# Optimization experiments

Hardware: AMD Instinct MI355X
Metric: run time of the kernel (lower is better)

## Reference

```python
import jax, jax.numpy as jnp
import numpy as np

N = 100000
E = 1600000
P = 500000
IN_C = 128
HID = 128


def _sage_conv(x, edge_index, w_l, b_l, w_r):
    # PyG SAGEConv (aggr='mean'): out = lin_l(mean_{j->i} x_j) + lin_r(x_i)
    src, dst = edge_index[0], edge_index[1]
    msg = x[src]                                    # [E, C] gather
    agg = jax.ops.segment_sum(msg, dst, num_segments=N)        # [N, C]
    deg = jax.ops.segment_sum(jnp.ones((src.shape[0],), x.dtype), dst, num_segments=N)
    mean = agg / jnp.clip(deg, 1.0)[:, None]
    return mean @ w_l + b_l + x @ w_r


def setup_inputs() -> dict:
    key = jax.random.key(0)
    ks = jax.random.split(key, 12)
    s_in = 1.0 / np.sqrt(IN_C)
    s_h = 1.0 / np.sqrt(HID)
    s_2h = 1.0 / np.sqrt(2 * HID)
    return {
        "x": jax.random.normal(ks[0], (N, IN_C), jnp.float32),
        "w1_l": jax.random.uniform(ks[1], (IN_C, HID), jnp.float32, -s_in, s_in),
        "b1": jax.random.uniform(ks[2], (HID,), jnp.float32, -s_in, s_in),
        "w1_r": jax.random.uniform(ks[3], (IN_C, HID), jnp.float32, -s_in, s_in),
        "w2_l": jax.random.uniform(ks[4], (HID, HID), jnp.float32, -s_h, s_h),
        "b2": jax.random.uniform(ks[5], (HID,), jnp.float32, -s_h, s_h),
        "w2_r": jax.random.uniform(ks[6], (HID, HID), jnp.float32, -s_h, s_h),
        "wd1": jax.random.uniform(ks[7], (2 * HID, HID), jnp.float32, -s_2h, s_2h),
        "bd1": jax.random.uniform(ks[8], (HID,), jnp.float32, -s_2h, s_2h),
        "wd2": jax.random.uniform(ks[9], (HID, 1), jnp.float32, -s_h, s_h),
        "bd2": jax.random.uniform(ks[10], (1,), jnp.float32, -s_h, s_h),
        "edge_index": jax.random.randint(ks[11], (2, E), 0, N, jnp.int64),
        "edge_pairs": jax.random.randint(jax.random.fold_in(key, 99), (2, P), 0, N, jnp.int64),
    }


def reference(x, w1_l, b1, w1_r, w2_l, b2, w2_r, wd1, bd1, wd2, bd2, edge_index, edge_pairs):
    # encode: two SAGEConv layers with ReLU between
    h = jax.nn.relu(_sage_conv(x, edge_index, w1_l, b1, w1_r))
    h = _sage_conv(h, edge_index, w2_l, b2, w2_r)
    # decode: gather endpoints, concat, 2-layer MLP, squeeze
    feat = jnp.concatenate([h[edge_pairs[0]], h[edge_pairs[1]]], axis=1)  # [P, 2H]
    out = jax.nn.relu(feat @ wd1 + bd1) @ wd2 + bd2
    return out.squeeze(-1)
```

## Files before the change

kernel.cpp:

```cpp
#include <hip/hip_runtime.h>
#include <hip/hip_bf16.h>

#define NN 100000
#define NE 1600000
#define NP 500000
#define C 128
#define NBUCK 782

typedef __attribute__((ext_vector_type(8))) short bf16x8;
typedef __attribute__((ext_vector_type(4))) float f32x4;
typedef _Float16 f16;
typedef __attribute__((ext_vector_type(4))) _Float16 f16x4;
typedef __attribute__((ext_vector_type(8))) _Float16 f16x8;

__device__ inline unsigned short bfbits(float x) {
    __hip_bfloat16 h = __float2bfloat16(x);
    union { __hip_bfloat16 h; unsigned short u; } v; v.h = h;
    return v.u;
}
__device__ inline float bf2f(unsigned short b) {
    return __uint_as_float(((unsigned)b) << 16);
}

__device__ inline void split8core(const float* xs, bf16x8& hi, bf16x8& lo) {
    union { unsigned short s[8]; bf16x8 v; } uh, ul;
#pragma unroll
    for (int j = 0; j < 8; ++j) {
        unsigned short h = bfbits(xs[j]);
        uh.s[j] = h;
        ul.s[j] = bfbits(xs[j] - bf2f(h));
    }
    hi = uh.v;
    lo = ul.v;
}

__device__ inline void split8(const float* p, bf16x8& hi, bf16x8& lo) {
    f32x4 a = *(const f32x4*)p;
    f32x4 b = *(const f32x4*)(p + 4);
    float xs[8] = {a.x, a.y, a.z, a.w, b.x, b.y, b.z, b.w};
    split8core(xs, hi, lo);
}

__device__ inline void split8h(const f16* p, bf16x8& hi, bf16x8& lo) {
    f16x8 v = *(const f16x8*)p;
    float xs[8];
#pragma unroll
    for (int j = 0; j < 8; ++j) xs[j] = (float)v[j];
    split8core(xs, hi, lo);
}

__global__ __launch_bounds__(256) void f32_to_f16_kernel(
        const float* __restrict__ in, f16* __restrict__ out, int n4) {
    int i = blockIdx.x * 256 + threadIdx.x;
    if (i < n4) {
        float4 v = *(const float4*)&in[i * 4];
        f16x4 h = {(f16)v.x, (f16)v.y, (f16)v.z, (f16)v.w};
        *(f16x4*)&out[i * 4] = h;
    }
}

__global__ __launch_bounds__(256) void bin_count_kernel(
        const int* __restrict__ dst, int* __restrict__ gcnt, int nE) {
    __shared__ int h[NBUCK];
    int tid = threadIdx.x;
    for (int i = tid; i < NBUCK; i += 256) h[i] = 0;
    __syncthreads();
    int base = blockIdx.x * 8192;
#pragma unroll
    for (int j = 0; j < 32; ++j) {
        int e = base + tid + j * 256;
        if (e < nE) atomicAdd(&h[dst[e] >> 7], 1);
    }
    __syncthreads();
    for (int i = tid; i < NBUCK; i += 256)
        if (h[i]) atomicAdd(&gcnt[i], h[i]);
}

__global__ __launch_bounds__(1024) void bin_scan_kernel(
        const int* __restrict__ gcnt, int* __restrict__ gstart,
        int* __restrict__ gcursor) {
    __shared__ int s[1024];
    int tid = threadIdx.x;
    int v = (tid < NBUCK) ? gcnt[tid] : 0;
    s[tid] = v;
    __syncthreads();
    for (int off = 1; off < 1024; off <<= 1) {
        int t = (tid >= off) ? s[tid - off] : 0;
        __syncthreads();
        s[tid] += t;
        __syncthreads();
    }
    int excl = s[tid] - v;
    if (tid < NBUCK) { gstart[tid] = excl; gcursor[tid] = excl; }
    if (tid == NBUCK - 1) gstart[NBUCK] = excl + v;
}

__global__ __launch_bounds__(256) void bin_scatter_kernel(
        const int* __restrict__ src, const int* __restrict__ dst,
        int* __restrict__ gcursor, unsigned* __restrict__ elist, int nE) {
    __shared__ unsigned stage[4096];
    __shared__ unsigned short sbkt[4096];
    __shared__ int h[NBUCK];
    __shared__ int ex[NBUCK];
    __shared__ int gb[NBUCK];
    __shared__ int psum[256];
    int tid = threadIdx.x;
    for (int i = tid; i < NBUCK; i += 256) h[i] = 0;
    __syncthreads();
    int base = blockIdx.x * 4096;
    unsigned pk[16]; int bk[16];
#pragma unroll
    for (int j = 0; j < 16; ++j) {
        int e = base + tid + j * 256;
        bool ok = e < nE;
        int d = ok ? dst[e] : 0;
        int s = ok ? src[e] : 0;
        bk[j] = ok ? (d >> 7) : -1;
        pk[j] = ((unsigned)(d & 127) << 17) | (unsigned)s;
        if (ok) atomicAdd(&h[bk[j]], 1);
    }
    __syncthreads();
    int lo = tid * 4;
    int c4[4]; int sum = 0;
#pragma unroll
    for (int j = 0; j < 4; ++j) {
        int idx = lo + j;
        c4[j] = (idx < NBUCK) ? h[idx] : 0;
        sum += c4[j];
    }
    psum[tid] = sum;
    __syncthreads();
    for (int off = 1; off < 256; off <<= 1) {
        int t = (tid >= off) ? psum[tid - off] : 0;
        __syncthreads();
        psum[tid] += t;
        __syncthreads();
    }
    int run = psum[tid] - sum;
#pragma unroll
    for (int j = 0; j < 4; ++j) {
        int idx = lo + j;
        if (idx < NBUCK) ex[idx] = run;
        run += c4[j];
    }
    __syncthreads();
    for (int i = tid; i < NBUCK; i += 256)
        if (h[i] > 0) gb[i] = atomicAdd(&gcursor[i], h[i]);
    for (int i = tid; i < NBUCK; i += 256) h[i] = 0;
    __syncthreads();
#pragma unroll
    for (int j = 0; j < 16; ++j) {
        if (bk[j] >= 0) {
            int r = ex[bk[j]] + atomicAdd(&h[bk[j]], 1);
            stage[r] = pk[j];
            sbkt[r] = (unsigned short)bk[j];
        }
    }
    __syncthreads();
    int tot = min(4096, nE - base);
    for (int i = tid; i < tot; i += 256) {
        int b = sbkt[i];
        elist[gb[b] + (i - ex[b])] = stage[i];
    }
}

__global__ __launch_bounds__(256) void bucket_csr_kernel(
        const unsigned* __restrict__ elist, const int* __restrict__ gstart,
        int* __restrict__ ssrc, int* __restrict__ offs) {
    __shared__ int cnt[128];
    __shared__ int sc[128];
    int tid = threadIdx.x;
    int b = blockIdx.x;
    if (tid < 128) cnt[tid] = 0;
    __syncthreads();
    int s = gstart[b], e = gstart[b + 1];
    for (int i = s + tid; i < e; i += 256)
        atomicAdd(&cnt[(elist[i] >> 17) & 127], 1);
    __syncthreads();
    int v = 0;
    if (tid < 128) { v = cnt[tid]; sc[tid] = v; }
    __syncthreads();
    for (int off = 1; off < 128; off <<= 1) {
        int t = 0;
        if (tid < 128 && tid >= off) t = sc[tid - off];
        __syncthreads();
        if (tid < 128) sc[tid] += t;
        __syncthreads();
    }
    if (tid < 128) {
        int start = s + sc[tid] - v;
        cnt[tid] = start;
        int node = b * 128 + tid;
        if (node < NN) offs[node] = start;
    }
    if (b == NBUCK - 1 && tid == 0) offs[NN] = NE;
    __syncthreads();
    for (int i = s + tid; i < e; i += 256) {
        unsigned p = elist[i];
        int r = (p >> 17) & 127;
        int pos = atomicAdd(&cnt[r], 1);
        ssrc[pos] = (int)(p & 0x1FFFF);
    }
}

__global__ void compose_kernel(const float* __restrict__ w2l, const float* __restrict__ w2r,
                               const float* __restrict__ b2,
                               const float* __restrict__ wd1, const float* __restrict__ bd1,
                               float* __restrict__ wcomp, float* __restrict__ bcomp) {
    int c = threadIdx.x;
    int k = blockIdx.x;
    if (k < C) {
        float wma = 0, wmb = 0, wha = 0, whb = 0;
        for (int j = 0; j < C; ++j) {
            float wt = wd1[j * C + c];
            float wb = wd1[(C + j) * C + c];
            float l = w2l[k * C + j];
            float r = w2r[k * C + j];
            wma += l * wt; wmb += l * wb;
            wha += r * wt; whb += r * wb;
        }
        wcomp[0 * C * C + k * C + c] = wma;
        wcomp[1 * C * C + k * C + c] = wha;
        wcomp[2 * C * C + k * C + c] = wmb;
        wcomp[3 * C * C + k * C + c] = whb;
    } else {
        float ba = bd1[c], bb = 0;
        for (int j = 0; j < C; ++j) {
            float bj = b2[j];
            ba += bj * wd1[j * C + c];
            bb += bj * wd1[(C + j) * C + c];
        }
        bcomp[c] = ba;
        bcomp[C + c] = bb;
    }
}

__global__ void pack_w1_kernel(const float* __restrict__ wl, const float* __restrict__ wr,
                               short* __restrict__ Wh, short* __restrict__ Wl) {
    int t = blockIdx.x * 256 + threadIdx.x;
    int j = t & 7, l = (t >> 3) & 63;
    int kf = (t >> 9) & 7;
    int nf = t >> 12;
    int k = kf * 32 + ((l >> 4) << 3) + j;
    int n = nf * 16 + (l & 15);
    float w = (k < C) ? wl[k * C + n] : wr[(k - C) * C + n];
    unsigned short h = bfbits(w);
    Wh[t] = (short)h;
    Wl[t] = (short)bfbits(w - bf2f(h));
}

__global__ void pack_w2_kernel(const float* __restrict__ wcomp,
                               short* __restrict__ Wh, short* __restrict__ Wl) {
    int t = blockIdx.x * 256 + threadIdx.x;
    int j = t & 7, l = (t >> 3) & 63;
    int kf = (t >> 9) & 7;
    int nf = t >> 12;
    int k = kf * 32 + ((l >> 4) << 3) + j;
    int n = nf * 16 + (l & 15);
    int sel = (k >= C ? 1 : 0) + (n >= C ? 2 : 0);
    float w = wcomp[sel * C * C + (k & (C - 1)) * C + (n & (C - 1))];
    unsigned short h = bfbits(w);
    Wh[t] = (short)h;
    Wl[t] = (short)bfbits(w - bf2f(h));
}

__global__ __launch_bounds__(256) void gather_mean_f16_kernel(
        const f16* __restrict__ xin, const int* __restrict__ offs,
        const int* __restrict__ ssrc, f16* __restrict__ mean) {
    int gid = blockIdx.x * 256 + threadIdx.x;
    int hw = gid >> 5;
    int lane = threadIdx.x & 31;
    int nhw = (gridDim.x * 256) >> 5;
    for (int n = hw; n < NN; n += nhw) {
        int start = offs[n];
        int end = offs[n + 1];
        float4 acc = make_float4(0.f, 0.f, 0.f, 0.f);
        int e = start;
        for (; e + 7 < end; e += 8) {
            f16x4 v[8];
#pragma unroll
            for (int u = 0; u < 8; ++u)
                v[u] = *(const f16x4*)(xin + (size_t)ssrc[e + u] * C + lane * 4);
#pragma unroll
            for (int u = 0; u < 8; ++u) {
                acc.x += (float)v[u][0]; acc.y += (float)v[u][1];
                acc.z += (float)v[u][2]; acc.w += (float)v[u][3];
            }
        }
        for (; e < end; ++e) {
            f16x4 v = *(const f16x4*)(xin + (size_t)ssrc[e] * C + lane * 4);
            acc.x += (float)v[0]; acc.y += (float)v[1];
            acc.z += (float)v[2]; acc.w += (float)v[3];
        }
        float inv = 1.0f / fmaxf((float)(end - start), 1.0f);
        f16x4 m = {(f16)(acc.x * inv), (f16)(acc.y * inv),
                   (f16)(acc.z * inv), (f16)(acc.w * inv)};
        *(f16x4*)(mean + (size_t)n * C + lane * 4) = m;
    }
}

template<int MS, int NF, int RELU, int A1F16>
__global__ __launch_bounds__(256, 4) void mfma_transform_kernel(
        const f16* A0, const void* A1v,
        const short* __restrict__ Bh, const short* __restrict__ Bl,
        const float* __restrict__ bias,
        f16* O0, f16* O1) {
    constexpr int KF = 8;
    int tid = threadIdx.x;
    int w = tid >> 6, l = tid & 63;
    int m0 = blockIdx.x * (64 * MS) + w * (MS * 16);
    int lr = l & 15;
    int lk = (l >> 4) * 8;

    f32x4 acc[MS][NF];
#pragma unroll
    for (int ms = 0; ms < MS; ++ms)
#pragma unroll
        for (int nf = 0; nf < NF; ++nf)
            acc[ms][nf] = (f32x4){0.0f, 0.0f, 0.0f, 0.0f};

    const bf16x8* Bhp = (const bf16x8*)Bh;
    const bf16x8* Blp = (const bf16x8*)Bl;

#pragma unroll
    for (int kf = 0; kf < KF; ++kf) {
        int kofs = (kf & 3) * 32 + lk;
        bf16x8 ah[MS], al[MS];
#pragma unroll
        for (int ms = 0; ms < MS; ++ms) {
            int r = m0 + ms * 16 + lr;
            r = (r < NN) ? r : (NN - 1);
            if (kf < 4) {
                split8h(A0 + (size_t)r * C + kofs, ah[ms], al[ms]);
            } else if (A1F16) {
                split8h((const f16*)A1v + (size_t)r * C + kofs, ah[ms], al[ms]);
            } else {
                split8((const float*)A1v + (size_t)r * C + kofs, ah[ms], al[ms]);
            }
        }
#pragma unroll
        for (int nf = 0; nf < NF; ++nf) {
            bf16x8 bh = Bhp[(nf * KF + kf) * 64 + l];
            bf16x8 bl = Blp[(nf * KF + kf) * 64 + l];
#pragma unroll
            for (int ms = 0; ms < MS; ++ms) {
                acc[ms][nf] = __builtin_amdgcn_mfma_f32_16x16x32_bf16(ah[ms], bh, acc[ms][nf], 0, 0, 0);
                acc[ms][nf] = __builtin_amdgcn_mfma_f32_16x16x32_bf16(al[ms], bh, acc[ms][nf], 0, 0, 0);
                acc[ms][nf] = __builtin_amdgcn_mfma_f32_16x16x32_bf16(ah[ms], bl, acc[ms][nf], 0, 0, 0);
            }
        }
    }

#pragma unroll
    for (int nf = 0; nf < NF; ++nf) {
        int col = nf * 16 + lr;
        float bv = bias[col];
        f16* O = (NF == 8) ? O0 : ((nf < 8) ? O0 : O1);
        int c = (nf & 7) * 16 + lr;
#pragma unroll
        for (int ms = 0; ms < MS; ++ms) {
#pragma unroll
            for (int i = 0; i < 4; ++i) {
                int r = m0 + ms * 16 + (l >> 4) * 4 + i;
                if (r < NN) {
                    float v = acc[ms][nf][i] + bv;
                    if (RELU) v = fmaxf(v, 0.0f);
                    O[(size_t)r * C + c] = (f16)v;
                }
            }
        }
    }
}

__global__ __launch_bounds__(256) void decode_kernel(
        const f16* __restrict__ a, const f16* __restrict__ b,
        const int* __restrict__ pu, const int* __restrict__ pv,
        const float* __restrict__ wd2, const float* __restrict__ bd2,
        float* __restrict__ out) {
    int gid = blockIdx.x * 256 + threadIdx.x;
    int hw = gid >> 5;
    int lane = threadIdx.x & 31;
    int nhw = (gridDim.x * 256) >> 5;
    float4 w2 = *(const float4*)&wd2[lane * 4];
    float bout = bd2[0];
    for (int p = hw; p < NP; p += 2 * nhw) {
        int p2 = p + nhw;
        bool ok2 = p2 < NP;
        int u1 = pu[p], v1 = pv[p];
        int u2 = ok2 ? pu[p2] : 0, v2 = ok2 ? pv[p2] : 0;
        f16x4 a1 = *(const f16x4*)(a + (size_t)u1 * C + lane * 4);
        f16x4 b1 = *(const f16x4*)(b + (size_t)v1 * C + lane * 4);
        f16x4 a2 = *(const f16x4*)(a + (size_t)u2 * C + lane * 4);
        f16x4 b2 = *(const f16x4*)(b + (size_t)v2 * C + lane * 4);
        float s1 = fmaxf((float)a1[0] + (float)b1[0], 0.0f) * w2.x
                 + fmaxf((float)a1[1] + (float)b1[1], 0.0f) * w2.y
                 + fmaxf((float)a1[2] + (float)b1[2], 0.0f) * w2.z
                 + fmaxf((float)a1[3] + (float)b1[3], 0.0f) * w2.w;
        float s2 = fmaxf((float)a2[0] + (float)b2[0], 0.0f) * w2.x
                 + fmaxf((float)a2[1] + (float)b2[1], 0.0f) * w2.y
                 + fmaxf((float)a2[2] + (float)b2[2], 0.0f) * w2.z
                 + fmaxf((float)a2[3] + (float)b2[3], 0.0f) * w2.w;
#pragma unroll
        for (int off = 16; off; off >>= 1) {
            s1 += __shfl_down(s1, off, 32);
            s2 += __shfl_down(s2, off, 32);
        }
        if (lane == 0) {
            out[p] = s1 + bout;
            if (ok2) out[p2] = s2 + bout;
        }
    }
}

extern "C" void kernel_launch(void* const* d_in, const int* in_sizes, int n_in,
                              void* d_out, int out_size, void* d_ws, size_t ws_size,
                              hipStream_t stream) {
    const float* x    = (const float*)d_in[0];
    const float* w1_l = (const float*)d_in[1];
    const float* b1   = (const float*)d_in[2];
    const float* w1_r = (const float*)d_in[3];
    const float* w2_l = (const float*)d_in[4];
    const float* b2   = (const float*)d_in[5];
    const float* w2_r = (const float*)d_in[6];
    const float* wd1  = (const float*)d_in[7];
    const float* bd1  = (const float*)d_in[8];
    const float* wd2  = (const float*)d_in[9];
    const float* bd2  = (const float*)d_in[10];
    const int* edge_index = (const int*)d_in[11];
    const int* edge_pairs = (const int*)d_in[12];

    const int* esrc = edge_index;
    const int* edst = edge_index + NE;
    const int* pu = edge_pairs;
    const int* pv = edge_pairs + NP;

    int* gcnt    = (int*)d_ws;
    int* gstart  = gcnt + 1024;
    int* gcursor = gstart + 1024;
    int* offs    = gcursor + 1024;
    unsigned* elist = (unsigned*)(offs + ((NN + 1 + 255) & ~255));
    int* ssrc    = (int*)(elist + NE);
    f16* xh      = (f16*)(ssrc + ((NE + 255) & ~255));
    f16* mean_h  = xh + (size_t)NN * C;
    f16* h1h     = mean_h + (size_t)NN * C;
    f16* a_h     = h1h + (size_t)NN * C;
    f16* b_h     = a_h + (size_t)NN * C;
    float* wcomp = (float*)(b_h + (size_t)NN * C);
    float* bcomp = wcomp + 4 * C * C;
    short* w1h = (short*)(bcomp + 2 * C);
    short* w1l = w1h + 256 * 128;
    short* w2h = w1l + 256 * 128;
    short* w2l = w2h + 256 * 256;

    hipMemsetAsync(gcnt, 0, sizeof(int) * 1024, stream);

    bin_count_kernel<<<(NE + 8191) / 8192, 256, 0, stream>>>(edst, gcnt, NE);
    bin_scan_kernel<<<1, 1024, 0, stream>>>(gcnt, gstart, gcursor);
    bin_scatter_kernel<<<(NE + 4095) / 4096, 256, 0, stream>>>(esrc, edst, gcursor, elist, NE);
    bucket_csr_kernel<<<NBUCK, 256, 0, stream>>>(elist, gstart, ssrc, offs);

    compose_kernel<<<C + 1, C, 0, stream>>>(w2_l, w2_r, b2, wd1, bd1, wcomp, bcomp);
    pack_w1_kernel<<<128, 256, 0, stream>>>(w1_l, w1_r, w1h, w1l);
    pack_w2_kernel<<<256, 256, 0, stream>>>(wcomp, w2h, w2l);

    f32_to_f16_kernel<<<(NN * C / 4 + 255) / 256, 256, 0, stream>>>(x, xh, NN * C / 4);

    gather_mean_f16_kernel<<<6144, 256, 0, stream>>>(xh, offs, ssrc, mean_h);
    mfma_transform_kernel<2, 8, 1, 0><<<(NN + 127) / 128, 256, 0, stream>>>(
        mean_h, (const void*)x, w1h, w1l, b1, h1h, nullptr);
    gather_mean_f16_kernel<<<6144, 256, 0, stream>>>(h1h, offs, ssrc, mean_h);
    mfma_transform_kernel<1, 16, 0, 1><<<(NN + 63) / 64, 256, 0, stream>>>(
        mean_h, (const void*)h1h, w2h, w2l, bcomp, a_h, b_h);

    decode_kernel<<<4096, 256, 0, stream>>>(a_h, b_h, pu, pv, wd2, bd2, (float*)d_out);
}
```

Measured before the change: 380.1 us.

## Switch transform GEMMs to f16 MFMA with split weights and 2D tiling

The dense transform kernels now feed the f16 activations straight into f16 MFMA instructions, dropping the per-element bf16 hi/lo split of the A operand. Only the weights keep a hi/lo f16 split, so each tile issues two MFMAs instead of three. The first layer reads the f16 copy of x instead of the f32 input. The tiling also changes to 4 row fragments by 4 column fragments per wave, with the output columns spread across blockIdx.y. This cuts ALU conversion work and MFMA count, but it re-reads the A rows once per column block and loses the lo-part correction on activations, which may affect accuracy.

```diff
diff --git a/kernel.cpp b/kernel.cpp
--- a/kernel.cpp
+++ b/kernel.cpp
@@ -7,47 +7,10 @@
 #define C 128
 #define NBUCK 782
 
-typedef __attribute__((ext_vector_type(8))) short bf16x8;
 typedef __attribute__((ext_vector_type(4))) float f32x4;
 typedef _Float16 f16;
 typedef __attribute__((ext_vector_type(4))) _Float16 f16x4;
 typedef __attribute__((ext_vector_type(8))) _Float16 f16x8;
-
-__device__ inline unsigned short bfbits(float x) {
-    __hip_bfloat16 h = __float2bfloat16(x);
-    union { __hip_bfloat16 h; unsigned short u; } v; v.h = h;
-    return v.u;
-}
-__device__ inline float bf2f(unsigned short b) {
-    return __uint_as_float(((unsigned)b) << 16);
-}
-
-__device__ inline void split8core(const float* xs, bf16x8& hi, bf16x8& lo) {
-    union { unsigned short s[8]; bf16x8 v; } uh, ul;
-#pragma unroll
-    for (int j = 0; j < 8; ++j) {
-        unsigned short h = bfbits(xs[j]);
-        uh.s[j] = h;
-        ul.s[j] = bfbits(xs[j] - bf2f(h));
-    }
-    hi = uh.v;
-    lo = ul.v;
-}
-
-__device__ inline void split8(const float* p, bf16x8& hi, bf16x8& lo) {
-    f32x4 a = *(const f32x4*)p;
-    f32x4 b = *(const f32x4*)(p + 4);
-    float xs[8] = {a.x, a.y, a.z, a.w, b.x, b.y, b.z, b.w};
-    split8core(xs, hi, lo);
-}
-
-__device__ inline void split8h(const f16* p, bf16x8& hi, bf16x8& lo) {
-    f16x8 v = *(const f16x8*)p;
-    float xs[8];
-#pragma unroll
-    for (int j = 0; j < 8; ++j) xs[j] = (float)v[j];
-    split8core(xs, hi, lo);
-}
 
 __global__ __launch_bounds__(256) void f32_to_f16_kernel(
         const float* __restrict__ in, f16* __restrict__ out, int n4) {
@@ -236,7 +199,7 @@
 }
 
 __global__ void pack_w1_kernel(const float* __restrict__ wl, const float* __restrict__ wr,
-                               short* __restrict__ Wh, short* __restrict__ Wl) {
+                               f16* __restrict__ Wh, f16* __restrict__ Wl) {
     int t = blockIdx.x * 256 + threadIdx.x;
     int j = t & 7, l = (t >> 3) & 63;
     int kf = (t >> 9) & 7;
@@ -244,13 +207,13 @@
     int k = kf * 32 + ((l >> 4) << 3) + j;
     int n = nf * 16 + (l & 15);
     float w = (k < C) ? wl[k * C + n] : wr[(k - C) * C + n];
-    unsigned short h = bfbits(w);
-    Wh[t] = (short)h;
-    Wl[t] = (short)bfbits(w - bf2f(h));
+    f16 h = (f16)w;
+    Wh[t] = h;
+    Wl[t] = (f16)(w - (float)h);
 }
 
 __global__ void pack_w2_kernel(const float* __restrict__ wcomp,
-                               short* __restrict__ Wh, short* __restrict__ Wl) {
+                               f16* __restrict__ Wh, f16* __restrict__ Wl) {
     int t = blockIdx.x * 256 + threadIdx.x;
     int j = t & 7, l = (t >> 3) & 63;
     int kf = (t >> 9) & 7;
@@ -259,9 +222,9 @@
     int n = nf * 16 + (l & 15);
     int sel = (k >= C ? 1 : 0) + (n >= C ? 2 : 0);
     float w = wcomp[sel * C * C + (k & (C - 1)) * C + (n & (C - 1))];
-    unsigned short h = bfbits(w);
-    Wh[t] = (short)h;
-    Wl[t] = (short)bfbits(w - bf2f(h));
+    f16 h = (f16)w;
+    Wh[t] = h;
+    Wl[t] = (f16)(w - (float)h);
 }
 
 __global__ __launch_bounds__(256) void gather_mean_f16_kernel(
@@ -299,16 +262,19 @@
     }
 }
 
-template<int MS, int NF, int RELU, int A1F16>
-__global__ __launch_bounds__(256, 4) void mfma_transform_kernel(
-        const f16* A0, const void* A1v,
-        const short* __restrict__ Bh, const short* __restrict__ Bl,
+template<int NFT, int RELU>
+__global__ __launch_bounds__(256, 4) void mfma_transform_f16_kernel(
+        const f16* __restrict__ A0, const f16* __restrict__ A1,
+        const f16* __restrict__ Bh, const f16* __restrict__ Bl,
         const float* __restrict__ bias,
         f16* O0, f16* O1) {
     constexpr int KF = 8;
+    constexpr int MS = 4;
+    constexpr int NF = 4;
     int tid = threadIdx.x;
     int w = tid >> 6, l = tid & 63;
     int m0 = blockIdx.x * (64 * MS) + w * (MS * 16);
+    int nf0 = blockIdx.y * NF;
     int lr = l & 15;
     int lk = (l >> 4) * 8;
 
@@ -319,44 +285,38 @@
         for (int nf = 0; nf < NF; ++nf)
             acc[ms][nf] = (f32x4){0.0f, 0.0f, 0.0f, 0.0f};
 
-    const bf16x8* Bhp = (const bf16x8*)Bh;
-    const bf16x8* Blp = (const bf16x8*)Bl;
+    const f16x8* Bhp = (const f16x8*)Bh;
+    const f16x8* Blp = (const f16x8*)Bl;
 
 #pragma unroll
     for (int kf = 0; kf < KF; ++kf) {
+        const f16* Asrc = (kf < 4) ? A0 : A1;
         int kofs = (kf & 3) * 32 + lk;
-        bf16x8 ah[MS], al[MS];
+        f16x8 a[MS];
 #pragma unroll
         for (int ms = 0; ms < MS; ++ms) {
             int r = m0 + ms * 16 + lr;
             r = (r < NN) ? r : (NN - 1);
-            if (kf < 4) {
-                split8h(A0 + (size_t)r * C + kofs, ah[ms], al[ms]);
-            } else if (A1F16) {
-                split8h((const f16*)A1v + (size_t)r * C + kofs, ah[ms], al[ms]);
-            } else {
-                split8((const float*)A1v + (size_t)r * C + kofs, ah[ms], al[ms]);
+            a[ms] = *(const f16x8*)(Asrc + (size_t)r * C + kofs);
+        }
+#pragma unroll
+        for (int nf = 0; nf < NF; ++nf) {
+            f16x8 bh = Bhp[((nf0 + nf) * KF + kf) * 64 + l];
+            f16x8 bl = Blp[((nf0 + nf) * KF + kf) * 64 + l];
+#pragma unroll
+            for (int ms = 0; ms < MS; ++ms) {
+                acc[ms][nf] = __builtin_amdgcn_mfma_f32_16x16x32_f16(a[ms], bh, acc[ms][nf], 0, 0, 0);
+                acc[ms][nf] = __builtin_amdgcn_mfma_f32_16x16x32_f16(a[ms], bl, acc[ms][nf], 0, 0, 0);
             }
         }
-#pragma unroll
-        for (int nf = 0; nf < NF; ++nf) {
-            bf16x8 bh = Bhp[(nf * KF + kf) * 64 + l];
-            bf16x8 bl = Blp[(nf * KF + kf) * 64 + l];
-#pragma unroll
-            for (int ms = 0; ms < MS; ++ms) {
-                acc[ms][nf] = __builtin_amdgcn_mfma_f32_16x16x32_bf16(ah[ms], bh, acc[ms][nf], 0, 0, 0);
-                acc[ms][nf] = __builtin_amdgcn_mfma_f32_16x16x32_bf16(al[ms], bh, acc[ms][nf], 0, 0, 0);
-                acc[ms][nf] = __builtin_amdgcn_mfma_f32_16x16x32_bf16(ah[ms], bl, acc[ms][nf], 0, 0, 0);
-            }
-        }
     }
 
 #pragma unroll
     for (int nf = 0; nf < NF; ++nf) {
-        int col = nf * 16 + lr;
-        float bv = bias[col];
-        f16* O = (NF == 8) ? O0 : ((nf < 8) ? O0 : O1);
-        int c = (nf & 7) * 16 + lr;
+        int nfg = nf0 + nf;
+        float bv = bias[nfg * 16 + lr];
+        f16* O = (NFT == 8) ? O0 : ((nfg < 8) ? O0 : O1);
+        int c = ((NFT == 8) ? nfg : (nfg & 7)) * 16 + lr;
 #pragma unroll
         for (int ms = 0; ms < MS; ++ms) {
 #pragma unroll
@@ -447,10 +407,10 @@
     f16* b_h     = a_h + (size_t)NN * C;
     float* wcomp = (float*)(b_h + (size_t)NN * C);
     float* bcomp = wcomp + 4 * C * C;
-    short* w1h = (short*)(bcomp + 2 * C);
-    short* w1l = w1h + 256 * 128;
-    short* w2h = w1l + 256 * 128;
-    short* w2l = w2h + 256 * 256;
+    f16* w1h = (f16*)(bcomp + 2 * C);
+    f16* w1l = w1h + 256 * 128;
+    f16* w2h = w1l + 256 * 128;
+    f16* w2l = w2h + 256 * 256;
 
     hipMemsetAsync(gcnt, 0, sizeof(int) * 1024, stream);
 
@@ -465,12 +425,13 @@
 
     f32_to_f16_kernel<<<(NN * C / 4 + 255) / 256, 256, 0, stream>>>(x, xh, NN * C / 4);
 
+    int rblocks = (NN + 255) / 256;
     gather_mean_f16_kernel<<<6144, 256, 0, stream>>>(xh, offs, ssrc, mean_h);
-    mfma_transform_kernel<2, 8, 1, 0><<<(NN + 127) / 128, 256, 0, stream>>>(
-        mean_h, (const void*)x, w1h, w1l, b1, h1h, nullptr);
+    mfma_transform_f16_kernel<8, 1><<<dim3(rblocks, 2), 256, 0, stream>>>(
+        mean_h, xh, w1h, w1l, b1, h1h, nullptr);
     gather_mean_f16_kernel<<<6144, 256, 0, stream>>>(h1h, offs, ssrc, mean_h);
-    mfma_transform_kernel<1, 16, 0, 1><<<(NN + 63) / 64, 256, 0, stream>>>(
-        mean_h, (const void*)h1h, w2h, w2l, bcomp, a_h, b_h);
+    mfma_transform_f16_kernel<16, 0><<<dim3(rblocks, 4), 256, 0, stream>>>(
+        mean_h, h1h, w2h, w2l, bcomp, a_h, b_h);
 
     decode_kernel<<<4096, 256, 0, stream>>>(a_h, b_h, pu, pv, wd2, bd2, (float*)d_out);
 }
```

After: 353.8 us. -6.9%, faster.
